# Kernel tuning notes

Measured on AMD Instinct MI355X. Metric: run time of the kernel, lower is better.

Reference implementation:

```python
import jax, jax.numpy as jnp
import numpy as np
import math

B, Q, K, D = 32, 2048, 2048, 128


def setup_inputs() -> dict:
    key = jax.random.key(0)
    k1, k2, k3, k4 = jax.random.split(key, 4)
    return {
        "queries": jax.random.normal(k1, (B, Q, D), dtype=jnp.float32),
        "keys": jax.random.normal(k2, (B, K, D), dtype=jnp.float32),
        "values": jax.random.normal(k3, (B, K, D), dtype=jnp.float32),
        "valid_len": jax.random.randint(k4, (B,), 0, Q, dtype=jnp.int32),
    }


def reference(queries, keys, values, valid_len):
    d = queries.shape[-1]
    # [B, Q, K] scores
    scores = jnp.einsum("bqd,bkd->bqk", queries, keys) / math.sqrt(d)
    # Faithful to source: mask is over the QUERY dim (X.size(1) of [B,Q,K]);
    # rows with q >= valid_len[b] are set entirely to -1e5 before softmax.
    row_mask = jnp.arange(scores.shape[1]) < valid_len[:, None]  # [B, Q]
    scores = jnp.where(row_mask[:, :, None], scores, -100000.0)
    attn = jax.nn.softmax(scores, axis=-1)  # dropout p=0 -> identity
    return jnp.einsum("bqk,bkv->bqv", attn, values)
```

## Files before the change

### kernel.cpp

```cpp
#include <hip/hip_runtime.h>
#include <stdint.h>

#define NB 32
#define NQ 2048
#define NKK 2048
#define DH 128

constexpr int QBLK = 128;
constexpr int KBLK = 64;
constexpr int NKT  = NKK / KBLK;
constexpr float C2 = 0.12754299817f;

typedef short short8  __attribute__((ext_vector_type(8)));
typedef float f32x4   __attribute__((ext_vector_type(4)));
typedef float f32x16  __attribute__((ext_vector_type(16)));
typedef uint32_t u32x4 __attribute__((ext_vector_type(4)));

typedef __attribute__((address_space(3))) uint32_t lds_u32_t;
typedef __attribute__((address_space(1))) const uint32_t glb_u32_t;

__device__ __forceinline__ uint16_t f2bf(float x) {
    union { float f; uint32_t u; } v; v.f = x;
    uint32_t r = v.u + 0x7fffu + ((v.u >> 16) & 1u);
    return (uint16_t)(r >> 16);
}

__device__ __forceinline__ void gload16(const void* g, void* l) {
    __builtin_amdgcn_global_load_lds((glb_u32_t*)g, (lds_u32_t*)l, 16, 0, 0);
}

__device__ __forceinline__ uint32_t cvtpk(float lo, float hi) {
    uint32_t d;
    asm("v_cvt_pk_bf16_f32 %0, %1, %2" : "=v"(d) : "v"(lo), "v"(hi));
    return d;
}

__global__ void conv_kf(const float* __restrict__ K, uint16_t* __restrict__ Kf) {
    __shared__ __align__(16) uint16_t T[64][136];
    const int bid = blockIdx.x;
    const int b = bid >> 5, kt = bid & 31;
    const int tid = threadIdx.x;
    const float* src = K + ((size_t)(b * NKK + kt * 64)) * DH;
    #pragma unroll
    for (int r = 0; r < 8; ++r) {
        int flat = r * 256 + tid;
        int row = flat >> 5;
        int c4 = (flat & 31) * 4;
        f32x4 x = *(const f32x4*)(src + (size_t)row * DH + c4);
        T[row][c4 + 0] = f2bf(x[0]);
        T[row][c4 + 1] = f2bf(x[1]);
        T[row][c4 + 2] = f2bf(x[2]);
        T[row][c4 + 3] = f2bf(x[3]);
    }
    __syncthreads();
    uint16_t* dst = Kf + (size_t)bid * 8192;
    #pragma unroll
    for (int r = 0; r < 4; ++r) {
        int c = r * 256 + tid;
        int s = c >> 6, lane = c & 63;
        int ci = s >> 3, t = s & 7;
        int mm = lane & 31, hh = lane >> 5;
        short8 v = *(const short8*)&T[ci * 32 + mm][t * 16 + hh * 8];
        *(short8*)(dst + (size_t)c * 8) = v;
    }
}

__global__ void conv_vf(const float* __restrict__ V, uint16_t* __restrict__ Vf) {
    const int bid = blockIdx.x;
    const int b = bid >> 5, kt = bid & 31;
    const int tid = threadIdx.x;
    const float* src = V + (size_t)b * NKK * DH;
    uint16_t* dst = Vf + (size_t)bid * 8192;
    #pragma unroll
    for (int r = 0; r < 4; ++r) {
        int c = r * 256 + tid;
        int s = c >> 6, lane = c & 63;
        int ci = s >> 3, nt = (s >> 1) & 3, uu = s & 1;
        int m = lane & 31, h = lane >> 5;
        int kb = kt * 64 + ci * 32 + uu * 16 + 4 * h;
        int d = nt * 32 + m;
        short8 w;
        #pragma unroll
        for (int j = 0; j < 8; ++j) {
            int key = kb + (j & 3) + 8 * (j >> 2);
            w[j] = (short)f2bf(src[(size_t)key * DH + d]);
        }
        *(short8*)(dst + (size_t)c * 8) = w;
    }
}

__global__ __launch_bounds__(256, 2)
void attn_fwd(const float* __restrict__ Qg, const uint16_t* __restrict__ Kf,
              const uint16_t* __restrict__ Vf, const int* __restrict__ VL,
              float* __restrict__ Og) {
    __shared__ __align__(16) uint8_t LB[65536];

    const int tid  = threadIdx.x;
    const int wv   = tid >> 6;
    const int lane = tid & 63;
    const int m    = lane & 31;
    const int h    = lane >> 5;

    const int bid = blockIdx.x;
    const int swz = (bid & 7) * 64 + (bid >> 3);
    const int b   = swz >> 4;
    const int qt  = swz & 15;
    const int qb0 = qt * QBLK + wv * 32;

    const int vlen = VL[b];
    const float sc = ((qb0 + m) < vlen) ? C2 : 0.0f;

    short8 qf[8];
    {
        const float* qp = Qg + ((size_t)b * NQ + qb0 + m) * DH;
        #pragma unroll
        for (int t = 0; t < 8; ++t) {
            const float* p = qp + t * 16 + h * 8;
            f32x4 x0 = *(const f32x4*)(p);
            f32x4 x1 = *(const f32x4*)(p + 4);
            short8 f;
            f[0] = f2bf(x0[0]); f[1] = f2bf(x0[1]); f[2] = f2bf(x0[2]); f[3] = f2bf(x0[3]);
            f[4] = f2bf(x1[0]); f[5] = f2bf(x1[1]); f[6] = f2bf(x1[2]); f[7] = f2bf(x1[3]);
            qf[t] = f;
        }
    }

    f32x16 oacc[4];
    #pragma unroll
    for (int nt = 0; nt < 4; ++nt)
        #pragma unroll
        for (int r = 0; r < 16; ++r) oacc[nt][r] = 0.0f;
    float lsum = 0.0f;

    const char* kfb = (const char*)Kf + (size_t)b * 32 * 16384;
    const char* vfb = (const char*)Vf + (size_t)b * 32 * 16384;

    auto stage = [&](int buf, int ktile) {
        const char* ks = kfb + (size_t)ktile * 16384;
        const char* vs = vfb + (size_t)ktile * 16384;
        char* kd = (char*)LB + buf * 16384;
        char* vd = (char*)LB + 32768 + buf * 16384;
        #pragma unroll
        for (int r = 0; r < 4; ++r) {
            gload16(ks + r * 4096 + tid * 16, kd + r * 4096 + tid * 16);
            gload16(vs + r * 4096 + tid * 16, vd + r * 4096 + tid * 16);
        }
    };

    stage(0, 0);
    __syncthreads();

    int cur = 0;
    for (int kt = 0; kt < NKT; ++kt) {
        if (kt + 1 < NKT) stage(cur ^ 1, kt + 1);
        const char* KTc = (const char*)LB + cur * 16384 + (size_t)lane * 16;
        const char* VTc = (const char*)LB + 32768 + cur * 16384 + (size_t)lane * 16;

        f32x16 sacc[2];
        #pragma unroll
        for (int ci = 0; ci < 2; ++ci)
            #pragma unroll
            for (int r = 0; r < 16; ++r) sacc[ci][r] = 0.0f;
        #pragma unroll
        for (int ci = 0; ci < 2; ++ci) {
            #pragma unroll
            for (int t = 0; t < 8; ++t) {
                short8 kf = *(const short8*)(KTc + (ci * 8 + t) * 1024);
                sacc[ci] = __builtin_amdgcn_mfma_f32_32x32x16_bf16(kf, qf[t], sacc[ci], 0, 0, 0);
            }
        }

        short8 pa[4];
        #pragma unroll
        for (int u = 0; u < 4; ++u) {
            const int ci = u >> 1;
            const int r0 = (u & 1) * 8;
            float p[8];
            #pragma unroll
            for (int j = 0; j < 8; ++j)
                p[j] = __builtin_amdgcn_exp2f(sacc[ci][r0 + j] * sc);
            lsum += ((p[0] + p[1]) + (p[2] + p[3])) + ((p[4] + p[5]) + (p[6] + p[7]));
            union { uint32_t w[4]; short8 s; } pu;
            pu.w[0] = cvtpk(p[0], p[1]);
            pu.w[1] = cvtpk(p[2], p[3]);
            pu.w[2] = cvtpk(p[4], p[5]);
            pu.w[3] = cvtpk(p[6], p[7]);
            pa[u] = pu.s;
        }

        #pragma unroll
        for (int nt = 0; nt < 4; ++nt) {
            #pragma unroll
            for (int u = 0; u < 4; ++u) {
                const int ci = u >> 1;
                const int uu = u & 1;
                short8 vfr = *(const short8*)(VTc + (ci * 8 + nt * 2 + uu) * 1024);
                oacc[nt] = __builtin_amdgcn_mfma_f32_32x32x16_bf16(pa[u], vfr, oacc[nt], 0, 0, 0);
            }
        }

        __syncthreads();
        cur ^= 1;
    }

    float ltot = lsum + __shfl_xor(lsum, 32);
    float* op = Og + ((size_t)b * NQ + qb0) * DH;
    #pragma unroll
    for (int r = 0; r < 16; ++r) {
        const int qr = (r & 3) + 8 * (r >> 2) + 4 * h;
        float lv = __shfl(ltot, qr);
        float inv = 1.0f / lv;
        #pragma unroll
        for (int nt = 0; nt < 4; ++nt)
            op[(size_t)qr * DH + nt * 32 + m] = oacc[nt][r] * inv;
    }
}

extern "C" void kernel_launch(void* const* d_in, const int* in_sizes, int n_in,
                              void* d_out, int out_size, void* d_ws, size_t ws_size,
                              hipStream_t stream) {
    const float* q  = (const float*)d_in[0];
    const float* k  = (const float*)d_in[1];
    const float* v  = (const float*)d_in[2];
    const int*   vl = (const int*)d_in[3];
    float* out = (float*)d_out;

    uint16_t* Kf = (uint16_t*)d_ws;
    uint16_t* Vf = Kf + (size_t)NB * NKT * 8192;

    conv_kf<<<NB * NKT, 256, 0, stream>>>(k, Kf);
    conv_vf<<<NB * NKT, 256, 0, stream>>>(v, Vf);
    attn_fwd<<<NB * (NQ / QBLK), 256, 0, stream>>>(q, Kf, Vf, vl, out);
}
```

Baseline: 90.51 us.

## Double query rows per wave to reuse K/V LDS fragments across two MFMA tiles

```diff
diff --git a/kernel.cpp b/kernel.cpp
--- a/kernel.cpp
+++ b/kernel.cpp
@@ -6,7 +6,7 @@
 #define NKK 2048
 #define DH 128
 
-constexpr int QBLK = 128;
+constexpr int QBLK = 256;
 constexpr int KBLK = 64;
 constexpr int NKT  = NKK / KBLK;
 constexpr float C2 = 0.12754299817f;
@@ -89,7 +89,7 @@
     }
 }
 
-__global__ __launch_bounds__(256, 2)
+__global__ __launch_bounds__(256, 1)
 void attn_fwd(const float* __restrict__ Qg, const uint16_t* __restrict__ Kf,
               const uint16_t* __restrict__ Vf, const int* __restrict__ VL,
               float* __restrict__ Og) {
@@ -102,35 +102,41 @@
     const int h    = lane >> 5;
 
     const int bid = blockIdx.x;
-    const int swz = (bid & 7) * 64 + (bid >> 3);
-    const int b   = swz >> 4;
-    const int qt  = swz & 15;
-    const int qb0 = qt * QBLK + wv * 32;
+    const int swz = (bid & 7) * 32 + (bid >> 3);
+    const int b   = swz >> 3;
+    const int qt  = swz & 7;
+    const int qb0 = qt * QBLK + wv * 64;
 
     const int vlen = VL[b];
-    const float sc = ((qb0 + m) < vlen) ? C2 : 0.0f;
-
-    short8 qf[8];
-    {
-        const float* qp = Qg + ((size_t)b * NQ + qb0 + m) * DH;
+
+    short8 qf[2][8];
+    #pragma unroll
+    for (int qs = 0; qs < 2; ++qs) {
+        const int qrow = qb0 + qs * 32 + m;
+        const float qsc = (qrow < vlen) ? C2 : 0.0f;
+        const float* qp = Qg + ((size_t)b * NQ + qrow) * DH;
         #pragma unroll
         for (int t = 0; t < 8; ++t) {
             const float* p = qp + t * 16 + h * 8;
             f32x4 x0 = *(const f32x4*)(p);
             f32x4 x1 = *(const f32x4*)(p + 4);
             short8 f;
-            f[0] = f2bf(x0[0]); f[1] = f2bf(x0[1]); f[2] = f2bf(x0[2]); f[3] = f2bf(x0[3]);
-            f[4] = f2bf(x1[0]); f[5] = f2bf(x1[1]); f[6] = f2bf(x1[2]); f[7] = f2bf(x1[3]);
-            qf[t] = f;
-        }
-    }
-
-    f32x16 oacc[4];
-    #pragma unroll
-    for (int nt = 0; nt < 4; ++nt)
-        #pragma unroll
-        for (int r = 0; r < 16; ++r) oacc[nt][r] = 0.0f;
-    float lsum = 0.0f;
+            f[0] = f2bf(x0[0] * qsc); f[1] = f2bf(x0[1] * qsc);
+            f[2] = f2bf(x0[2] * qsc); f[3] = f2bf(x0[3] * qsc);
+            f[4] = f2bf(x1[0] * qsc); f[5] = f2bf(x1[1] * qsc);
+            f[6] = f2bf(x1[2] * qsc); f[7] = f2bf(x1[3] * qsc);
+            qf[qs][t] = f;
+        }
+    }
+
+    f32x16 oacc[2][4];
+    #pragma unroll
+    for (int qs = 0; qs < 2; ++qs)
+        #pragma unroll
+        for (int nt = 0; nt < 4; ++nt)
+            #pragma unroll
+            for (int r = 0; r < 16; ++r) oacc[qs][nt][r] = 0.0f;
+    float lsum[2] = {0.0f, 0.0f};
 
     const char* kfb = (const char*)Kf + (size_t)b * 32 * 16384;
     const char* vfb = (const char*)Vf + (size_t)b * 32 * 16384;
@@ -156,36 +162,36 @@
         const char* KTc = (const char*)LB + cur * 16384 + (size_t)lane * 16;
         const char* VTc = (const char*)LB + 32768 + cur * 16384 + (size_t)lane * 16;
 
-        f32x16 sacc[2];
-        #pragma unroll
-        for (int ci = 0; ci < 2; ++ci)
-            #pragma unroll
-            for (int r = 0; r < 16; ++r) sacc[ci][r] = 0.0f;
+        short8 pa[2][4];
         #pragma unroll
         for (int ci = 0; ci < 2; ++ci) {
+            f32x16 s0, s1;
+            #pragma unroll
+            for (int r = 0; r < 16; ++r) { s0[r] = 0.0f; s1[r] = 0.0f; }
             #pragma unroll
             for (int t = 0; t < 8; ++t) {
                 short8 kf = *(const short8*)(KTc + (ci * 8 + t) * 1024);
-                sacc[ci] = __builtin_amdgcn_mfma_f32_32x32x16_bf16(kf, qf[t], sacc[ci], 0, 0, 0);
+                s0 = __builtin_amdgcn_mfma_f32_32x32x16_bf16(kf, qf[0][t], s0, 0, 0, 0);
+                s1 = __builtin_amdgcn_mfma_f32_32x32x16_bf16(kf, qf[1][t], s1, 0, 0, 0);
             }
-        }
-
-        short8 pa[4];
-        #pragma unroll
-        for (int u = 0; u < 4; ++u) {
-            const int ci = u >> 1;
-            const int r0 = (u & 1) * 8;
-            float p[8];
-            #pragma unroll
-            for (int j = 0; j < 8; ++j)
-                p[j] = __builtin_amdgcn_exp2f(sacc[ci][r0 + j] * sc);
-            lsum += ((p[0] + p[1]) + (p[2] + p[3])) + ((p[4] + p[5]) + (p[6] + p[7]));
-            union { uint32_t w[4]; short8 s; } pu;
-            pu.w[0] = cvtpk(p[0], p[1]);
-            pu.w[1] = cvtpk(p[2], p[3]);
-            pu.w[2] = cvtpk(p[4], p[5]);
-            pu.w[3] = cvtpk(p[6], p[7]);
-            pa[u] = pu.s;
+            #pragma unroll
+            for (int uu = 0; uu < 2; ++uu) {
+                float p0[8], p1[8];
+                #pragma unroll
+                for (int j = 0; j < 8; ++j) {
+                    p0[j] = __builtin_amdgcn_exp2f(s0[uu * 8 + j]);
+                    p1[j] = __builtin_amdgcn_exp2f(s1[uu * 8 + j]);
+                }
+                lsum[0] += ((p0[0] + p0[1]) + (p0[2] + p0[3])) + ((p0[4] + p0[5]) + (p0[6] + p0[7]));
+                lsum[1] += ((p1[0] + p1[1]) + (p1[2] + p1[3])) + ((p1[4] + p1[5]) + (p1[6] + p1[7]));
+                union { uint32_t w[4]; short8 s; } u0, u1;
+                u0.w[0] = cvtpk(p0[0], p0[1]); u0.w[1] = cvtpk(p0[2], p0[3]);
+                u0.w[2] = cvtpk(p0[4], p0[5]); u0.w[3] = cvtpk(p0[6], p0[7]);
+                u1.w[0] = cvtpk(p1[0], p1[1]); u1.w[1] = cvtpk(p1[2], p1[3]);
+                u1.w[2] = cvtpk(p1[4], p1[5]); u1.w[3] = cvtpk(p1[6], p1[7]);
+                pa[0][ci * 2 + uu] = u0.s;
+                pa[1][ci * 2 + uu] = u1.s;
+            }
         }
 
         #pragma unroll
@@ -195,7 +201,8 @@
                 const int ci = u >> 1;
                 const int uu = u & 1;
                 short8 vfr = *(const short8*)(VTc + (ci * 8 + nt * 2 + uu) * 1024);
-                oacc[nt] = __builtin_amdgcn_mfma_f32_32x32x16_bf16(pa[u], vfr, oacc[nt], 0, 0, 0);
+                oacc[0][nt] = __builtin_amdgcn_mfma_f32_32x32x16_bf16(pa[0][u], vfr, oacc[0][nt], 0, 0, 0);
+                oacc[1][nt] = __builtin_amdgcn_mfma_f32_32x32x16_bf16(pa[1][u], vfr, oacc[1][nt], 0, 0, 0);
             }
         }
 
@@ -203,16 +210,20 @@
         cur ^= 1;
     }
 
-    float ltot = lsum + __shfl_xor(lsum, 32);
+    float lt0 = lsum[0] + __shfl_xor(lsum[0], 32);
+    float lt1 = lsum[1] + __shfl_xor(lsum[1], 32);
     float* op = Og + ((size_t)b * NQ + qb0) * DH;
     #pragma unroll
-    for (int r = 0; r < 16; ++r) {
-        const int qr = (r & 3) + 8 * (r >> 2) + 4 * h;
-        float lv = __shfl(ltot, qr);
-        float inv = 1.0f / lv;
-        #pragma unroll
-        for (int nt = 0; nt < 4; ++nt)
-            op[(size_t)qr * DH + nt * 32 + m] = oacc[nt][r] * inv;
+    for (int qs = 0; qs < 2; ++qs) {
+        float ltq = qs ? lt1 : lt0;
+        #pragma unroll
+        for (int r = 0; r < 16; ++r) {
+            const int qr = (r & 3) + 8 * (r >> 2) + 4 * h;
+            float inv = 1.0f / __shfl(ltq, qr);
+            #pragma unroll
+            for (int nt = 0; nt < 4; ++nt)
+                op[(size_t)(qs * 32 + qr) * DH + nt * 32 + m] = oacc[qs][nt][r] * inv;
+        }
     }
 }
 
```

New measurement: 94.76 us. +4.7%, slower.

## Read V fragments directly from global, fold scale into Q, add setprio

Applied to the files above, without the earlier changes.

```diff
diff --git a/kernel.cpp b/kernel.cpp
--- a/kernel.cpp
+++ b/kernel.cpp
@@ -93,11 +93,11 @@
 void attn_fwd(const float* __restrict__ Qg, const uint16_t* __restrict__ Kf,
               const uint16_t* __restrict__ Vf, const int* __restrict__ VL,
               float* __restrict__ Og) {
-    __shared__ __align__(16) uint8_t LB[65536];
+    __shared__ __align__(16) uint8_t LB[32768];
 
     const int tid  = threadIdx.x;
+    const int lane = tid & 63;
     const int wv   = tid >> 6;
-    const int lane = tid & 63;
     const int m    = lane & 31;
     const int h    = lane >> 5;
 
@@ -108,19 +108,22 @@
     const int qb0 = qt * QBLK + wv * 32;
 
     const int vlen = VL[b];
-    const float sc = ((qb0 + m) < vlen) ? C2 : 0.0f;
+    const int qrow = qb0 + m;
+    const float qsc = (qrow < vlen) ? C2 : 0.0f;
 
     short8 qf[8];
     {
-        const float* qp = Qg + ((size_t)b * NQ + qb0 + m) * DH;
+        const float* qp = Qg + ((size_t)b * NQ + qrow) * DH;
         #pragma unroll
         for (int t = 0; t < 8; ++t) {
             const float* p = qp + t * 16 + h * 8;
             f32x4 x0 = *(const f32x4*)(p);
             f32x4 x1 = *(const f32x4*)(p + 4);
             short8 f;
-            f[0] = f2bf(x0[0]); f[1] = f2bf(x0[1]); f[2] = f2bf(x0[2]); f[3] = f2bf(x0[3]);
-            f[4] = f2bf(x1[0]); f[5] = f2bf(x1[1]); f[6] = f2bf(x1[2]); f[7] = f2bf(x1[3]);
+            f[0] = f2bf(x0[0] * qsc); f[1] = f2bf(x0[1] * qsc);
+            f[2] = f2bf(x0[2] * qsc); f[3] = f2bf(x0[3] * qsc);
+            f[4] = f2bf(x1[0] * qsc); f[5] = f2bf(x1[1] * qsc);
+            f[6] = f2bf(x1[2] * qsc); f[7] = f2bf(x1[3] * qsc);
             qf[t] = f;
         }
     }
@@ -137,14 +140,10 @@
 
     auto stage = [&](int buf, int ktile) {
         const char* ks = kfb + (size_t)ktile * 16384;
-        const char* vs = vfb + (size_t)ktile * 16384;
         char* kd = (char*)LB + buf * 16384;
-        char* vd = (char*)LB + 32768 + buf * 16384;
-        #pragma unroll
-        for (int r = 0; r < 4; ++r) {
+        #pragma unroll
+        for (int r = 0; r < 4; ++r)
             gload16(ks + r * 4096 + tid * 16, kd + r * 4096 + tid * 16);
-            gload16(vs + r * 4096 + tid * 16, vd + r * 4096 + tid * 16);
-        }
     };
 
     stage(0, 0);
@@ -154,21 +153,22 @@
     for (int kt = 0; kt < NKT; ++kt) {
         if (kt + 1 < NKT) stage(cur ^ 1, kt + 1);
         const char* KTc = (const char*)LB + cur * 16384 + (size_t)lane * 16;
-        const char* VTc = (const char*)LB + 32768 + cur * 16384 + (size_t)lane * 16;
+        const char* VTc = vfb + (size_t)kt * 16384 + (size_t)lane * 16;
 
         f32x16 sacc[2];
         #pragma unroll
         for (int ci = 0; ci < 2; ++ci)
             #pragma unroll
             for (int r = 0; r < 16; ++r) sacc[ci][r] = 0.0f;
-        #pragma unroll
-        for (int ci = 0; ci < 2; ++ci) {
-            #pragma unroll
-            for (int t = 0; t < 8; ++t) {
-                short8 kf = *(const short8*)(KTc + (ci * 8 + t) * 1024);
-                sacc[ci] = __builtin_amdgcn_mfma_f32_32x32x16_bf16(kf, qf[t], sacc[ci], 0, 0, 0);
-            }
-        }
+        __builtin_amdgcn_s_setprio(1);
+        #pragma unroll
+        for (int t = 0; t < 8; ++t) {
+            short8 kf0 = *(const short8*)(KTc + (0 * 8 + t) * 1024);
+            short8 kf1 = *(const short8*)(KTc + (1 * 8 + t) * 1024);
+            sacc[0] = __builtin_amdgcn_mfma_f32_32x32x16_bf16(kf0, qf[t], sacc[0], 0, 0, 0);
+            sacc[1] = __builtin_amdgcn_mfma_f32_32x32x16_bf16(kf1, qf[t], sacc[1], 0, 0, 0);
+        }
+        __builtin_amdgcn_s_setprio(0);
 
         short8 pa[4];
         #pragma unroll
@@ -178,7 +178,7 @@
             float p[8];
             #pragma unroll
             for (int j = 0; j < 8; ++j)
-                p[j] = __builtin_amdgcn_exp2f(sacc[ci][r0 + j] * sc);
+                p[j] = __builtin_amdgcn_exp2f(sacc[ci][r0 + j]);
             lsum += ((p[0] + p[1]) + (p[2] + p[3])) + ((p[4] + p[5]) + (p[6] + p[7]));
             union { uint32_t w[4]; short8 s; } pu;
             pu.w[0] = cvtpk(p[0], p[1]);
@@ -188,6 +188,7 @@
             pa[u] = pu.s;
         }
 
+        __builtin_amdgcn_s_setprio(1);
         #pragma unroll
         for (int nt = 0; nt < 4; ++nt) {
             #pragma unroll
@@ -198,6 +199,7 @@
                 oacc[nt] = __builtin_amdgcn_mfma_f32_32x32x16_bf16(pa[u], vfr, oacc[nt], 0, 0, 0);
             }
         }
+        __builtin_amdgcn_s_setprio(0);
 
         __syncthreads();
         cur ^= 1;
```

Measured after the change: 151.3 us. 1.67x slower.
